# Optimization experiments

Hardware: AMD Instinct MI355X
Metric: run time of the kernel (lower is better)

## Reference

```python
import jax, jax.numpy as jnp
import numpy as np

T, B, C = 2048, 8, 512
OUT = 512
NE = 16
TOPK = 2
LOSS_SCALE = 0.01
NEG_INF = 1.0e6  # module uses -1000000.0 for masked logits


def setup_inputs() -> dict:
    key = jax.random.key(0)
    k = jax.random.split(key, 4)
    a_assign = np.sqrt(6.0 / (C + NE)).astype(np.float32)  # xavier_uniform for Linear(C, NE)
    a_w1 = np.float32(np.sqrt(6.0) / (C + OUT))            # dynamic_init_method == 1
    return {
        "x": jax.random.normal(k[0], (T, B, C), dtype=jnp.float32),
        "assign_w": jax.random.uniform(k[1], (NE, C), minval=-a_assign, maxval=a_assign, dtype=jnp.float32),
        "assign_b": jnp.zeros((NE,), dtype=jnp.float32),
        "pw_w1": jax.random.uniform(k[2], (NE, OUT * C), minval=-a_w1, maxval=a_w1, dtype=jnp.float32),
        "bias_w": jnp.zeros((OUT, C), dtype=jnp.float32),  # pw_bias weight initialized to 0
        "bias_b": jnp.zeros((OUT,), dtype=jnp.float32),
    }


def reference(x, assign_w, assign_b, pw_w1, bias_w, bias_b):
    # key=None path of ConditionalDLFactorized18.forward, eval mode, tau=0 -> softmax gating.
    tokens = x.reshape(T * B, C)
    # Gating energies: Linear(key_dim, ne)
    energies = tokens @ assign_w.T + assign_b  # [TB, ne]
    # keeptopk_masked: set entries below k-th largest to -1e6
    topv, _ = jax.lax.top_k(energies, TOPK)
    energies = jnp.where(energies < topv[..., TOPK - 1:TOPK], -NEG_INF, energies)
    resp = jax.nn.softmax(energies, axis=-1)  # [TB, ne]
    # Importance/commitment loss (torch.std is unbiased -> ddof=1)
    importance = resp.sum(axis=0)  # [ne]
    loss = (LOSS_SCALE * jnp.std(importance, ddof=1) / jnp.mean(importance)).reshape(1)
    # Algebraically-equivalent reorder of (resp @ pw_w1).view(T,B,out,in) @ x:
    # apply each expert's matrix to the token first, then mix with resp.
    W = pw_w1.reshape(NE, OUT, C)
    expert_out = jnp.einsum("nc,eoc->neo", tokens, W)      # [TB, ne, out]
    y = jnp.einsum("ne,neo->no", resp, expert_out)          # [TB, out]
    y = y.reshape(T, B, OUT)
    # dynamic bias: pw_bias(x0) = x0 @ bias_w.T + bias_b
    y = y + x @ bias_w.T + bias_b
    return y, loss
```

## Files before the change

### kernel.cpp

```cpp
#include <hip/hip_runtime.h>
#include <hip/hip_bf16.h>

#define TB 16384
#define CDIM 512
#define OUTD 512
#define NE 16
#define NE_TOT 17
#define LOSS_SCALE 0.01f
#define BM 256
#define BN 128
#define BK 32
#define NSTEP 16
#define MAX_SCHED 80
#define MAXFLAG 8192
#define MARGIN 1e-3f

typedef __bf16 bf16_t;
typedef bf16_t bf16x8 __attribute__((ext_vector_type(8)));
typedef float f32x4 __attribute__((ext_vector_type(4)));
typedef unsigned short ushort4_t __attribute__((ext_vector_type(4)));
typedef unsigned short ushort8_t __attribute__((ext_vector_type(8)));

__device__ __forceinline__ unsigned short f2bf(float f) {
    unsigned int u = __float_as_uint(f);
    u += 0x7fffu + ((u >> 16) & 1u);
    return (unsigned short)(u >> 16);
}
__device__ __forceinline__ float bf2f(unsigned short h) {
    return __uint_as_float((unsigned int)h << 16);
}
__device__ __forceinline__ int sw4(int r) { return (r ^ (r >> 2)) & 3; }

__device__ __forceinline__ void async_copy16(void* lds, const void* g) {
    __builtin_amdgcn_global_load_lds(
        (const __attribute__((address_space(1))) unsigned int*)g,
        (__attribute__((address_space(3))) unsigned int*)lds, 16, 0, 0);
}

__global__ __launch_bounds__(256) void k_prep(
    const float* __restrict__ aw, unsigned short* __restrict__ awhl,
    int* cnt0, int* cnt1, float* importance, int* nflag, int* wflag)
{
    int t = threadIdx.x;
    if (t < NE) { cnt0[t] = 0; cnt1[t] = 0; importance[t] = 0.f; }
    if (t == 0) { *nflag = 0; *wflag = 0; }
    for (int i = t; i < NE * CDIM; i += 256) {
        float f = aw[i];
        unsigned short h = f2bf(f);
        float r = f - bf2f(h);
        awhl[i] = h;
        awhl[NE * CDIM + i] = f2bf(r);
    }
}

__global__ void k_wconv(const float* __restrict__ pw, const float* __restrict__ bw,
                        unsigned short* __restrict__ wbf, int* __restrict__ wflag) {
    long i = (long)blockIdx.x * 256 + threadIdx.x;
    const long NPW = (long)NE * OUTD * CDIM / 4;
    const long NTOT = (long)NE_TOT * OUTD * CDIM / 4;
    if (i >= NTOT) return;
    const float* src = (i < NPW) ? (pw + i * 4) : (bw + (i - NPW) * 4);
    float4 v = *(const float4*)src;
    ushort4_t o;
    o[0] = f2bf(v.x); o[1] = f2bf(v.y); o[2] = f2bf(v.z); o[3] = f2bf(v.w);
    long row = i >> 7;
    int e0 = (int)(i & 127) * 4;
    int kt = e0 >> 5;
    int cc = (e0 >> 3) & 3;
    int half = e0 & 7;
    int ccs = cc ^ sw4((int)(row & 15));
    *(ushort4_t*)(wbf + row * CDIM + kt * 32 + ccs * 8 + half) = o;
    if (i >= NPW && (v.x != 0.f || v.y != 0.f || v.z != 0.f || v.w != 0.f))
        atomicOr(wflag, 1);
}

__global__ __launch_bounds__(256) void k_gate(
    const float* __restrict__ x, const unsigned short* __restrict__ awhl,
    const float* __restrict__ ab,
    int* __restrict__ dec, float2* __restrict__ respd,
    int* __restrict__ flaglist, int* __restrict__ nflag, float* __restrict__ importance)
{
    __shared__ float imp_s[NE];
    int tid = threadIdx.x;
    if (tid < NE) imp_s[tid] = 0.f;
    __syncthreads();

    int wv = tid >> 6, l = tid & 63;
    int n0 = blockIdx.x * 64 + wv * 16;
    int e = l & 15;
    int kg = l >> 4;

    const float* xrow = x + (size_t)(n0 + e) * CDIM + kg * 8;
    const unsigned short* whiP = awhl + e * CDIM + kg * 8;
    const unsigned short* wloP = whiP + NE * CDIM;

    f32x4 acc = (f32x4){0.f, 0.f, 0.f, 0.f};
    #pragma unroll 4
    for (int ks = 0; ks < 16; ++ks) {
        float4 v0 = *(const float4*)(xrow + ks * 32);
        float4 v1 = *(const float4*)(xrow + ks * 32 + 4);
        ushort8_t hx, lx;
        #define CVT(idx, f) { unsigned short h_ = f2bf(f); hx[idx] = h_; \
                              float r_ = (f) - bf2f(h_); lx[idx] = f2bf(r_); }
        CVT(0, v0.x) CVT(1, v0.y) CVT(2, v0.z) CVT(3, v0.w)
        CVT(4, v1.x) CVT(5, v1.y) CVT(6, v1.z) CVT(7, v1.w)
        #undef CVT
        ushort8_t wh8 = *(const ushort8_t*)(whiP + ks * 32);
        ushort8_t wl8 = *(const ushort8_t*)(wloP + ks * 32);
        bf16x8 ah = *(bf16x8*)&hx, al = *(bf16x8*)&lx;
        bf16x8 bh = *(bf16x8*)&wh8, bl = *(bf16x8*)&wl8;
        acc = __builtin_amdgcn_mfma_f32_16x16x32_bf16(al, bh, acc, 0, 0, 0);
        acc = __builtin_amdgcn_mfma_f32_16x16x32_bf16(ah, bl, acc, 0, 0, 0);
        acc = __builtin_amdgcn_mfma_f32_16x16x32_bf16(ah, bh, acc, 0, 0, 0);
    }
    float bias = ab[e];
    f32x4 E;
    #pragma unroll
    for (int q = 0; q < 4; ++q) E[q] = acc[q] + bias;

    f32x4 m1 = E, m2, m3;
    #pragma unroll
    for (int q = 0; q < 4; ++q) { m2[q] = -3.4e38f; m3[q] = -3.4e38f; }
    #pragma unroll
    for (int off = 1; off <= 8; off <<= 1) {
        #pragma unroll
        for (int q = 0; q < 4; ++q) {
            float o1 = __shfl_xor(m1[q], off, 64);
            float o2 = __shfl_xor(m2[q], off, 64);
            float o3 = __shfl_xor(m3[q], off, 64);
            float M1 = fmaxf(m1[q], o1), x1 = fminf(m1[q], o1);
            float h2 = fmaxf(m2[q], o2), l2 = fminf(m2[q], o2);
            float M2 = fmaxf(x1, h2), x2 = fminf(x1, h2);
            float M3 = fmaxf(fmaxf(x2, l2), fmaxf(m3[q], o3));
            m1[q] = M1; m2[q] = M2; m3[q] = M3;
        }
    }
    f32x4 p, z;
    #pragma unroll
    for (int q = 0; q < 4; ++q) p[q] = (E[q] >= m2[q]) ? expf(E[q] - m1[q]) : 0.f;
    z = p;
    #pragma unroll
    for (int off = 1; off <= 8; off <<= 1)
        #pragma unroll
        for (int q = 0; q < 4; ++q) z[q] += __shfl_xor(z[q], off, 64);
    f32x4 resp;
    #pragma unroll
    for (int q = 0; q < 4; ++q) resp[q] = p[q] / z[q];

    int grp = l >> 4;
    int elo_q[4], ehi_q[4];
    float rlo_q[4], rhi_q[4];
    #pragma unroll
    for (int q = 0; q < 4; ++q) {
        unsigned long long mq = __ballot(p[q] > 0.f);
        unsigned int sub = (unsigned int)((mq >> (grp * 16)) & 0xffffULL);
        elo_q[q] = __builtin_ctz(sub);
        ehi_q[q] = 31 - __builtin_clz(sub);
        rlo_q[q] = __shfl(resp[q], grp * 16 + elo_q[q], 64);
        rhi_q[q] = __shfl(resp[q], grp * 16 + ehi_q[q], 64);
    }
    if ((l & 15) == 0) {
        #pragma unroll
        for (int q = 0; q < 4; ++q) {
            int n = n0 + grp * 4 + q;
            dec[n] = elo_q[q] | (ehi_q[q] << 8);
            respd[n] = make_float2(rlo_q[q], rhi_q[q]);
            if (m2[q] - m3[q] < MARGIN) {
                int ix = atomicAdd(nflag, 1);
                if (ix < MAXFLAG) flaglist[ix] = n;
            }
        }
    }
    float s = resp[0] + resp[1] + resp[2] + resp[3];
    s += __shfl_xor(s, 16, 64);
    s += __shfl_xor(s, 32, 64);
    if (l < 16) atomicAdd(&imp_s[e], s);
    __syncthreads();
    if (tid < NE) unsafeAtomicAdd(&importance[tid], imp_s[tid]);
}

__global__ __launch_bounds__(256) void k_repair(
    const float* __restrict__ x, const float* __restrict__ aw, const float* __restrict__ ab,
    const int* __restrict__ flaglist, const int* __restrict__ nflag,
    int* __restrict__ dec, float2* __restrict__ respd, float* __restrict__ importance)
{
    __shared__ double part[16][17];
    __shared__ double Ed[16];
    int tid = threadIdx.x;
    int e = tid >> 4, p = tid & 15;
    int nf = *nflag; if (nf > MAXFLAG) nf = MAXFLAG;
    for (int fi = blockIdx.x; fi < nf; fi += gridDim.x) {
        int n = flaglist[fi];
        const float* xp_ = x + (size_t)n * CDIM + p * 32;
        const float* wp = aw + e * CDIM + p * 32;
        double acc = 0.0;
        for (int j = 0; j < 32; ++j) acc = fma((double)xp_[j], (double)wp[j], acc);
        part[e][p] = acc;
        __syncthreads();
        if (tid < 16) {
            double s = (double)ab[tid];
            for (int q = 0; q < 16; ++q) s += part[tid][q];
            Ed[tid] = s;
        }
        __syncthreads();
        if (tid == 0) {
            double m1 = -1e300, m2 = -1e300, m3 = -1e300;
            for (int q = 0; q < 16; ++q) {
                double v = Ed[q];
                if (v > m1) { m3 = m2; m2 = m1; m1 = v; }
                else if (v > m2) { m3 = m2; m2 = v; }
                else if (v > m3) { m3 = v; }
            }
            int elo = -1, ehi = -1;
            for (int q = 0; q < 16; ++q)
                if (Ed[q] >= m2) { if (elo < 0) elo = q; else ehi = q; }
            double plo = exp(Ed[elo] - m1), phi = exp(Ed[ehi] - m1);
            double zz = plo + phi;
            float rlo = (float)(plo / zz), rhi = (float)(phi / zz);
            int od = dec[n]; float2 orr = respd[n];
            unsafeAtomicAdd(&importance[od & 0xff], -orr.x);
            unsafeAtomicAdd(&importance[(od >> 8) & 0xff], -orr.y);
            unsafeAtomicAdd(&importance[elo], rlo);
            unsafeAtomicAdd(&importance[ehi], rhi);
            dec[n] = elo | (ehi << 8);
            respd[n] = make_float2(rlo, rhi);
        }
        __syncthreads();
    }
}

__global__ __launch_bounds__(256) void k_count(
    const int* __restrict__ dec, int* __restrict__ cnt0, int* __restrict__ cnt1)
{
    __shared__ int l0[NE], l1[NE];
    int tid = threadIdx.x;
    if (tid < NE) { l0[tid] = 0; l1[tid] = 0; }
    __syncthreads();
    int d = dec[blockIdx.x * 256 + tid];
    atomicAdd(&l0[d & 0xff], 1);
    atomicAdd(&l1[(d >> 8) & 0xff], 1);
    __syncthreads();
    if (tid < NE) {
        if (l0[tid]) atomicAdd(&cnt0[tid], l0[tid]);
        if (l1[tid]) atomicAdd(&cnt1[tid], l1[tid]);
    }
}

__global__ void k_finish(const float* __restrict__ importance, float* __restrict__ out_loss,
                         const int* __restrict__ cnt0, const int* __restrict__ cnt1,
                         int* __restrict__ fill0, int* __restrict__ fill1,
                         int* __restrict__ end0a, int* __restrict__ end1a,
                         int* __restrict__ sched0, int* __restrict__ sched1,
                         int* __restrict__ sn0, int* __restrict__ sn1) {
    int l = threadIdx.x;
    if (l < 64) {
        float v = (l < NE) ? importance[l] : 0.f;
        float s = v;
        #pragma unroll
        for (int off = 8; off >= 1; off >>= 1) s += __shfl_xor(s, off, 64);
        float mean = s / 16.f;
        float d = (l < NE) ? (v - mean) : 0.f;
        float ss = d * d;
        #pragma unroll
        for (int off = 8; off >= 1; off >>= 1) ss += __shfl_xor(ss, off, 64);
        if (l == 0) {
            float stdv = sqrtf(ss / 15.f);
            out_loss[0] = LOSS_SCALE * stdv / mean;
        }
    } else if (l == 64) {
        int p = 0, base = 0;
        for (int e = 0; e < NE; ++e) {
            fill0[e] = base;
            end0a[e] = base + cnt0[e];
            int nb = (cnt0[e] + BM - 1) / BM;
            for (int i = 0; i < nb; ++i) sched0[p++] = (e << 20) | (base + i * BM);
            base += cnt0[e];
        }
        *sn0 = p;
    } else if (l == 65) {
        int p = 0, base = 0;
        for (int e = 0; e < NE; ++e) {
            fill1[e] = base;
            end1a[e] = base + cnt1[e];
            int nb = (cnt1[e] + BM - 1) / BM;
            for (int i = 0; i < nb; ++i) sched1[p++] = (e << 20) | (base + i * BM);
            base += cnt1[e];
        }
        *sn1 = p;
    }
}

__global__ __launch_bounds__(256) void k_scatter(
    const int* __restrict__ dec, int* __restrict__ fill0, int* __restrict__ fill1,
    int* __restrict__ idx0c, int* __restrict__ idx1c)
{
    __shared__ int l0[NE], l1[NE], b0[NE], b1[NE];
    int tid = threadIdx.x;
    if (tid < NE) { l0[tid] = 0; l1[tid] = 0; }
    __syncthreads();
    int n = blockIdx.x * 256 + tid;
    int d = dec[n];
    int elo = d & 0xff, ehi = (d >> 8) & 0xff;
    int p0 = atomicAdd(&l0[elo], 1);
    int p1 = atomicAdd(&l1[ehi], 1);
    __syncthreads();
    if (tid < NE) {
        b0[tid] = atomicAdd(&fill0[tid], l0[tid]);
        b1[tid] = atomicAdd(&fill1[tid], l1[tid]);
    }
    __syncthreads();
    idx0c[b0[elo] + p0] = n;
    idx1c[b1[ehi] + p1] = n;
}

__global__ __launch_bounds__(256) void k_permute(
    const float* __restrict__ x, const int* __restrict__ idxc,
    unsigned short* __restrict__ xp)
{
    int slot = blockIdx.x * 4 + (threadIdx.x >> 6);
    int l = threadIdx.x & 63;
    int tok = idxc[slot];
    const float4* src = (const float4*)(x + (size_t)tok * CDIM);
    float4 v0 = src[2 * l];
    float4 v1 = src[2 * l + 1];
    ushort8_t h;
    h[0] = f2bf(v0.x); h[1] = f2bf(v0.y); h[2] = f2bf(v0.z); h[3] = f2bf(v0.w);
    h[4] = f2bf(v1.x); h[5] = f2bf(v1.y); h[6] = f2bf(v1.z); h[7] = f2bf(v1.w);
    *(ushort8_t*)(xp + (size_t)slot * CDIM + l * 8) = h;
}

template<int MODE>
__global__ __launch_bounds__(512) void k_gemm(
    const unsigned short* __restrict__ xp, const unsigned short* __restrict__ wbf,
    const int* __restrict__ idxc, const float2* __restrict__ respd,
    const int* __restrict__ sched, const int* __restrict__ sn,
    const int* __restrict__ enda, const int* __restrict__ wflag,
    const float* __restrict__ bias_b, float* __restrict__ y)
{
    int e, m0, end;
    if (MODE == 2) {
        if (*wflag == 0) return;
        e = NE; m0 = blockIdx.x * BM; end = TB;
    } else {
        if ((int)blockIdx.x >= *sn) return;
        int s = sched[blockIdx.x];
        e = s >> 20; m0 = s & 0xFFFFF; end = enda[e];
    }
    int n0 = blockIdx.y * BN;
    int tid = threadIdx.x;
    int wave = tid >> 6, lane = tid & 63;
    int wm = wave >> 1, wn = wave & 1;
    int fr = lane & 15, fq = lane >> 4;

    __shared__ unsigned short As[2][BM * BK];
    __shared__ unsigned short Bs[2][BN * BK];

    f32x4 acc[4][4];
    #pragma unroll
    for (int m = 0; m < 4; ++m)
        #pragma unroll
        for (int nn = 0; nn < 4; ++nn) acc[m][nn] = (f32x4){0.f, 0.f, 0.f, 0.f};

    int rl = lane >> 2, cc = lane & 3;
    const unsigned short* aS[2];
    #pragma unroll
    for (int c = 0; c < 2; ++c) {
        int rloc = wave * 32 + c * 16 + rl;
        int rr = m0 + rloc; if (rr >= end) rr = end - 1;
        aS[c] = xp + (size_t)rr * CDIM + (cc ^ sw4(rloc)) * 8;
    }
    const unsigned short* bS =
        wbf + ((size_t)e * OUTD + n0 + wave * 16 + rl) * CDIM + cc * 8;

    auto stage = [&](int buf, int t) {
        async_copy16(&As[buf][(wave * 32) * BK], aS[0] + t * BK);
        async_copy16(&As[buf][(wave * 32 + 16) * BK], aS[1] + t * BK);
        async_copy16(&Bs[buf][(wave * 16) * BK], bS + t * BK);
    };
    auto compute = [&](int cb) {
        bf16x8 af[4], bv[4];
        #pragma unroll
        for (int m = 0; m < 4; ++m) {
            int row = wm * 64 + m * 16 + fr;
            af[m] = *(const bf16x8*)(&As[cb][row * BK + ((fq ^ sw4(fr)) * 8)]);
        }
        #pragma unroll
        for (int nn = 0; nn < 4; ++nn) {
            int row = wn * 64 + nn * 16 + fr;
            bv[nn] = *(const bf16x8*)(&Bs[cb][row * BK + ((fq ^ sw4(fr)) * 8)]);
        }
        #pragma unroll
        for (int m = 0; m < 4; ++m)
            #pragma unroll
            for (int nn = 0; nn < 4; ++nn)
                acc[m][nn] = __builtin_amdgcn_mfma_f32_16x16x32_bf16(af[m], bv[nn], acc[m][nn], 0, 0, 0);
    };

    stage(0, 0); stage(1, 1);
    #pragma unroll
    for (int t = 0; t < NSTEP; ++t) {
        if (t < NSTEP - 1) asm volatile("s_waitcnt vmcnt(3)" ::: "memory");
        else               asm volatile("s_waitcnt vmcnt(0)" ::: "memory");
        __builtin_amdgcn_sched_barrier(0);
        __builtin_amdgcn_s_barrier();
        asm volatile("" ::: "memory");
        compute(t & 1);
        __builtin_amdgcn_s_barrier();
        asm volatile("" ::: "memory");
        if (t + 2 < NSTEP) stage(t & 1, t + 2);
    }

    float bb[4];
    if (MODE == 0) {
        #pragma unroll
        for (int nn = 0; nn < 4; ++nn) bb[nn] = bias_b[n0 + wn * 64 + nn * 16 + fr];
    }
    #pragma unroll
    for (int m = 0; m < 4; ++m)
        #pragma unroll
        for (int q = 0; q < 4; ++q) {
            int r = m0 + wm * 64 + m * 16 + fq * 4 + q;
            if (r < end) {
                int tok = idxc[r];
                float w = 1.f;
                if (MODE != 2) {
                    float2 rp = respd[tok];
                    w = (MODE == 0) ? rp.x : rp.y;
                }
                float* yrow = y + (size_t)tok * OUTD + n0 + wn * 64 + fr;
                #pragma unroll
                for (int nn = 0; nn < 4; ++nn) {
                    if (MODE == 0)      yrow[nn * 16] = fmaf(w, acc[m][nn][q], bb[nn]);
                    else if (MODE == 1) yrow[nn * 16] += w * acc[m][nn][q];
                    else                yrow[nn * 16] += acc[m][nn][q];
                }
            }
        }
}

extern "C" void kernel_launch(void* const* d_in, const int* in_sizes, int n_in,
                              void* d_out, int out_size, void* d_ws, size_t ws_size,
                              hipStream_t stream) {
    const float* x        = (const float*)d_in[0];
    const float* assign_w = (const float*)d_in[1];
    const float* assign_b = (const float*)d_in[2];
    const float* pw_w1    = (const float*)d_in[3];
    const float* bias_w   = (const float*)d_in[4];
    const float* bias_b   = (const float*)d_in[5];
    float* y    = (float*)d_out;
    float* loss = y + (size_t)TB * OUTD;

    char* ws = (char*)d_ws;
    unsigned short* wbf  = (unsigned short*)(ws);
    unsigned short* xp   = (unsigned short*)(ws + 8912896);
    int*    idx0c     = (int*)   (ws + 25952256);
    int*    idx1c     = (int*)   (ws + 26017792);
    int*    dec       = (int*)   (ws + 26083328);
    float2* respd     = (float2*)(ws + 26148864);
    int*    flaglist  = (int*)   (ws + 26279936);
    unsigned short* awhl = (unsigned short*)(ws + 26312704);
    char*   misc      = ws + 26345472;
    int*    cnt0      = (int*)   (misc + 0);
    int*    cnt1      = (int*)   (misc + 64);
    int*    fill0     = (int*)   (misc + 128);
    int*    fill1     = (int*)   (misc + 192);
    int*    end0a     = (int*)   (misc + 256);
    int*    end1a     = (int*)   (misc + 320);
    float*  importance= (float*) (misc + 384);
    int*    nflag     = (int*)   (misc + 448);
    int*    wflag     = (int*)   (misc + 452);
    int*    sn0       = (int*)   (misc + 456);
    int*    sn1       = (int*)   (misc + 460);
    int*    sched0    = (int*)   (misc + 512);
    int*    sched1    = (int*)   (misc + 832);

    k_prep<<<1, 256, 0, stream>>>(assign_w, awhl, cnt0, cnt1, importance, nflag, wflag);
    k_wconv<<<(NE_TOT * OUTD * CDIM / 4 + 255) / 256, 256, 0, stream>>>(pw_w1, bias_w, wbf, wflag);
    k_gate<<<TB / 64, 256, 0, stream>>>(x, awhl, assign_b, dec, respd,
                                        flaglist, nflag, importance);
    k_repair<<<32, 256, 0, stream>>>(x, assign_w, assign_b, flaglist, nflag,
                                     dec, respd, importance);
    k_count<<<TB / 256, 256, 0, stream>>>(dec, cnt0, cnt1);
    k_finish<<<1, 128, 0, stream>>>(importance, loss, cnt0, cnt1, fill0, fill1,
                                    end0a, end1a, sched0, sched1, sn0, sn1);
    k_scatter<<<TB / 256, 256, 0, stream>>>(dec, fill0, fill1, idx0c, idx1c);
    k_permute<<<TB / 4, 256, 0, stream>>>(x, idx0c, xp);
    k_gemm<0><<<dim3(MAX_SCHED, OUTD / BN), 512, 0, stream>>>(
        xp, wbf, idx0c, respd, sched0, sn0, end0a, wflag, bias_b, y);
    k_permute<<<TB / 4, 256, 0, stream>>>(x, idx1c, xp);
    k_gemm<1><<<dim3(MAX_SCHED, OUTD / BN), 512, 0, stream>>>(
        xp, wbf, idx1c, respd, sched1, sn1, end1a, wflag, bias_b, y);
    k_gemm<2><<<dim3(TB / BM, OUTD / BN), 512, 0, stream>>>(
        xp, wbf, idx1c, respd, sched1, sn1, end1a, wflag, bias_b, y);
}
```

Baseline: 128.8 us.

## Fuse bf16 token conversion and expert counting into gate; gather rows in GEMM

The gate kernel already converts each token to bf16 for the gating MFMA, so it now writes that bf16 copy of x to the workspace. The two per-expert permute kernels are removed, and the GEMM gathers token rows through the index list instead. Per-expert counts are accumulated in the gate kernel, and the repair kernel adjusts them when a token's expert changes, which removes the separate count kernel. This saves two full passes over x plus the conversion writes and one launch, at the cost of indirect, non-contiguous row loads in the GEMM A operand.

```diff
diff --git a/kernel.cpp b/kernel.cpp
--- a/kernel.cpp
+++ b/kernel.cpp
@@ -76,13 +76,15 @@
 
 __global__ __launch_bounds__(256) void k_gate(
     const float* __restrict__ x, const unsigned short* __restrict__ awhl,
-    const float* __restrict__ ab,
+    const float* __restrict__ ab, unsigned short* __restrict__ xbf,
     int* __restrict__ dec, float2* __restrict__ respd,
-    int* __restrict__ flaglist, int* __restrict__ nflag, float* __restrict__ importance)
+    int* __restrict__ flaglist, int* __restrict__ nflag, float* __restrict__ importance,
+    int* __restrict__ cnt0, int* __restrict__ cnt1)
 {
     __shared__ float imp_s[NE];
+    __shared__ int c0_s[NE], c1_s[NE];
     int tid = threadIdx.x;
-    if (tid < NE) imp_s[tid] = 0.f;
+    if (tid < NE) { imp_s[tid] = 0.f; c0_s[tid] = 0; c1_s[tid] = 0; }
     __syncthreads();
 
     int wv = tid >> 6, l = tid & 63;
@@ -91,6 +93,7 @@
     int kg = l >> 4;
 
     const float* xrow = x + (size_t)(n0 + e) * CDIM + kg * 8;
+    unsigned short* xbrow = xbf + (size_t)(n0 + e) * CDIM + kg * 8;
     const unsigned short* whiP = awhl + e * CDIM + kg * 8;
     const unsigned short* wloP = whiP + NE * CDIM;
 
@@ -105,6 +108,7 @@
         CVT(0, v0.x) CVT(1, v0.y) CVT(2, v0.z) CVT(3, v0.w)
         CVT(4, v1.x) CVT(5, v1.y) CVT(6, v1.z) CVT(7, v1.w)
         #undef CVT
+        *(ushort8_t*)(xbrow + ks * 32) = hx;
         ushort8_t wh8 = *(const ushort8_t*)(whiP + ks * 32);
         ushort8_t wl8 = *(const ushort8_t*)(wloP + ks * 32);
         bf16x8 ah = *(bf16x8*)&hx, al = *(bf16x8*)&lx;
@@ -165,6 +169,8 @@
             int n = n0 + grp * 4 + q;
             dec[n] = elo_q[q] | (ehi_q[q] << 8);
             respd[n] = make_float2(rlo_q[q], rhi_q[q]);
+            atomicAdd(&c0_s[elo_q[q]], 1);
+            atomicAdd(&c1_s[ehi_q[q]], 1);
             if (m2[q] - m3[q] < MARGIN) {
                 int ix = atomicAdd(nflag, 1);
                 if (ix < MAXFLAG) flaglist[ix] = n;
@@ -176,13 +182,18 @@
     s += __shfl_xor(s, 32, 64);
     if (l < 16) atomicAdd(&imp_s[e], s);
     __syncthreads();
-    if (tid < NE) unsafeAtomicAdd(&importance[tid], imp_s[tid]);
+    if (tid < NE) {
+        unsafeAtomicAdd(&importance[tid], imp_s[tid]);
+        if (c0_s[tid]) atomicAdd(&cnt0[tid], c0_s[tid]);
+        if (c1_s[tid]) atomicAdd(&cnt1[tid], c1_s[tid]);
+    }
 }
 
 __global__ __launch_bounds__(256) void k_repair(
     const float* __restrict__ x, const float* __restrict__ aw, const float* __restrict__ ab,
     const int* __restrict__ flaglist, const int* __restrict__ nflag,
-    int* __restrict__ dec, float2* __restrict__ respd, float* __restrict__ importance)
+    int* __restrict__ dec, float2* __restrict__ respd, float* __restrict__ importance,
+    int* __restrict__ cnt0, int* __restrict__ cnt1)
 {
     __shared__ double part[16][17];
     __shared__ double Ed[16];
@@ -218,31 +229,17 @@
             double zz = plo + phi;
             float rlo = (float)(plo / zz), rhi = (float)(phi / zz);
             int od = dec[n]; float2 orr = respd[n];
-            unsafeAtomicAdd(&importance[od & 0xff], -orr.x);
-            unsafeAtomicAdd(&importance[(od >> 8) & 0xff], -orr.y);
+            int oelo = od & 0xff, oehi = (od >> 8) & 0xff;
+            unsafeAtomicAdd(&importance[oelo], -orr.x);
+            unsafeAtomicAdd(&importance[oehi], -orr.y);
             unsafeAtomicAdd(&importance[elo], rlo);
             unsafeAtomicAdd(&importance[ehi], rhi);
+            if (oelo != elo) { atomicSub(&cnt0[oelo], 1); atomicAdd(&cnt0[elo], 1); }
+            if (oehi != ehi) { atomicSub(&cnt1[oehi], 1); atomicAdd(&cnt1[ehi], 1); }
             dec[n] = elo | (ehi << 8);
             respd[n] = make_float2(rlo, rhi);
         }
         __syncthreads();
-    }
-}
-
-__global__ __launch_bounds__(256) void k_count(
-    const int* __restrict__ dec, int* __restrict__ cnt0, int* __restrict__ cnt1)
-{
-    __shared__ int l0[NE], l1[NE];
-    int tid = threadIdx.x;
-    if (tid < NE) { l0[tid] = 0; l1[tid] = 0; }
-    __syncthreads();
-    int d = dec[blockIdx.x * 256 + tid];
-    atomicAdd(&l0[d & 0xff], 1);
-    atomicAdd(&l1[(d >> 8) & 0xff], 1);
-    __syncthreads();
-    if (tid < NE) {
-        if (l0[tid]) atomicAdd(&cnt0[tid], l0[tid]);
-        if (l1[tid]) atomicAdd(&cnt1[tid], l1[tid]);
     }
 }
 
@@ -313,25 +310,9 @@
     idx1c[b1[ehi] + p1] = n;
 }
 
-__global__ __launch_bounds__(256) void k_permute(
-    const float* __restrict__ x, const int* __restrict__ idxc,
-    unsigned short* __restrict__ xp)
-{
-    int slot = blockIdx.x * 4 + (threadIdx.x >> 6);
-    int l = threadIdx.x & 63;
-    int tok = idxc[slot];
-    const float4* src = (const float4*)(x + (size_t)tok * CDIM);
-    float4 v0 = src[2 * l];
-    float4 v1 = src[2 * l + 1];
-    ushort8_t h;
-    h[0] = f2bf(v0.x); h[1] = f2bf(v0.y); h[2] = f2bf(v0.z); h[3] = f2bf(v0.w);
-    h[4] = f2bf(v1.x); h[5] = f2bf(v1.y); h[6] = f2bf(v1.z); h[7] = f2bf(v1.w);
-    *(ushort8_t*)(xp + (size_t)slot * CDIM + l * 8) = h;
-}
-
 template<int MODE>
 __global__ __launch_bounds__(512) void k_gemm(
-    const unsigned short* __restrict__ xp, const unsigned short* __restrict__ wbf,
+    const unsigned short* __restrict__ xbf, const unsigned short* __restrict__ wbf,
     const int* __restrict__ idxc, const float2* __restrict__ respd,
     const int* __restrict__ sched, const int* __restrict__ sn,
     const int* __restrict__ enda, const int* __restrict__ wflag,
@@ -366,8 +347,10 @@
     #pragma unroll
     for (int c = 0; c < 2; ++c) {
         int rloc = wave * 32 + c * 16 + rl;
-        int rr = m0 + rloc; if (rr >= end) rr = end - 1;
-        aS[c] = xp + (size_t)rr * CDIM + (cc ^ sw4(rloc)) * 8;
+        int tokr;
+        if (MODE == 2) tokr = m0 + rloc;
+        else { int rr = m0 + rloc; if (rr >= end) rr = end - 1; tokr = idxc[rr]; }
+        aS[c] = xbf + (size_t)tokr * CDIM + (cc ^ sw4(rloc)) * 8;
     }
     const unsigned short* bS =
         wbf + ((size_t)e * OUTD + n0 + wave * 16 + rl) * CDIM + cc * 8;
@@ -421,7 +404,7 @@
         for (int q = 0; q < 4; ++q) {
             int r = m0 + wm * 64 + m * 16 + fq * 4 + q;
             if (r < end) {
-                int tok = idxc[r];
+                int tok = (MODE == 2) ? r : idxc[r];
                 float w = 1.f;
                 if (MODE != 2) {
                     float2 rp = respd[tok];
@@ -452,14 +435,14 @@
 
     char* ws = (char*)d_ws;
     unsigned short* wbf  = (unsigned short*)(ws);
-    unsigned short* xp   = (unsigned short*)(ws + 8912896);
-    int*    idx0c     = (int*)   (ws + 25952256);
-    int*    idx1c     = (int*)   (ws + 26017792);
-    int*    dec       = (int*)   (ws + 26083328);
-    float2* respd     = (float2*)(ws + 26148864);
-    int*    flaglist  = (int*)   (ws + 26279936);
-    unsigned short* awhl = (unsigned short*)(ws + 26312704);
-    char*   misc      = ws + 26345472;
+    unsigned short* xbf  = (unsigned short*)(ws + 8912896);
+    int*    idx0c     = (int*)   (ws + 25690112);
+    int*    idx1c     = (int*)   (ws + 25755648);
+    int*    dec       = (int*)   (ws + 25821184);
+    float2* respd     = (float2*)(ws + 25886720);
+    int*    flaglist  = (int*)   (ws + 26017792);
+    unsigned short* awhl = (unsigned short*)(ws + 26050560);
+    char*   misc      = ws + 26083328;
     int*    cnt0      = (int*)   (misc + 0);
     int*    cnt1      = (int*)   (misc + 64);
     int*    fill0     = (int*)   (misc + 128);
@@ -476,20 +459,17 @@
 
     k_prep<<<1, 256, 0, stream>>>(assign_w, awhl, cnt0, cnt1, importance, nflag, wflag);
     k_wconv<<<(NE_TOT * OUTD * CDIM / 4 + 255) / 256, 256, 0, stream>>>(pw_w1, bias_w, wbf, wflag);
-    k_gate<<<TB / 64, 256, 0, stream>>>(x, awhl, assign_b, dec, respd,
-                                        flaglist, nflag, importance);
+    k_gate<<<TB / 64, 256, 0, stream>>>(x, awhl, assign_b, xbf, dec, respd,
+                                        flaglist, nflag, importance, cnt0, cnt1);
     k_repair<<<32, 256, 0, stream>>>(x, assign_w, assign_b, flaglist, nflag,
-                                     dec, respd, importance);
-    k_count<<<TB / 256, 256, 0, stream>>>(dec, cnt0, cnt1);
+                                     dec, respd, importance, cnt0, cnt1);
     k_finish<<<1, 128, 0, stream>>>(importance, loss, cnt0, cnt1, fill0, fill1,
                                     end0a, end1a, sched0, sched1, sn0, sn1);
     k_scatter<<<TB / 256, 256, 0, stream>>>(dec, fill0, fill1, idx0c, idx1c);
-    k_permute<<<TB / 4, 256, 0, stream>>>(x, idx0c, xp);
     k_gemm<0><<<dim3(MAX_SCHED, OUTD / BN), 512, 0, stream>>>(
-        xp, wbf, idx0c, respd, sched0, sn0, end0a, wflag, bias_b, y);
-    k_permute<<<TB / 4, 256, 0, stream>>>(x, idx1c, xp);
+        xbf, wbf, idx0c, respd, sched0, sn0, end0a, wflag, bias_b, y);
     k_gemm<1><<<dim3(MAX_SCHED, OUTD / BN), 512, 0, stream>>>(
-        xp, wbf, idx1c, respd, sched1, sn1, end1a, wflag, bias_b, y);
+        xbf, wbf, idx1c, respd, sched1, sn1, end1a, wflag, bias_b, y);
     k_gemm<2><<<dim3(TB / BM, OUTD / BN), 512, 0, stream>>>(
-        xp, wbf, idx1c, respd, sched1, sn1, end1a, wflag, bias_b, y);
-}
+        xbf, wbf, idx1c, respd, sched1, sn1, end1a, wflag, bias_b, y);
+}
```

New measurement: 111.5 us. 1.16x faster.
